# Optimization experiments

Hardware: AMD Instinct MI355X
Metric: run time of the kernel (lower is better)

## Reference

```python
import jax, jax.numpy as jnp
import numpy as np

H = 256  # GRU hidden size (self.dim)

def setup_inputs() -> dict:
    key = jax.random.key(0)
    ks = jax.random.split(key, 7)
    B, T, N_IN, N_C = 256, 512, 512, 101
    s_ih = 1.0 / np.sqrt(H)
    x    = jax.random.normal(ks[0], (B, T, N_IN), dtype=jnp.float32)
    W_ih = jax.random.uniform(ks[1], (3 * H, N_IN), minval=-s_ih, maxval=s_ih, dtype=jnp.float32)
    W_hh = jax.random.uniform(ks[2], (3 * H, H),    minval=-s_ih, maxval=s_ih, dtype=jnp.float32)
    b_ih = jax.random.uniform(ks[3], (3 * H,), minval=-s_ih, maxval=s_ih, dtype=jnp.float32)
    b_hh = jax.random.uniform(ks[4], (3 * H,), minval=-s_ih, maxval=s_ih, dtype=jnp.float32)
    s_fc = 1.0 / np.sqrt(H)
    fc_w = jax.random.uniform(ks[5], (N_C, H), minval=-s_fc, maxval=s_fc, dtype=jnp.float32)
    fc_b = jax.random.uniform(ks[6], (N_C,),   minval=-s_fc, maxval=s_fc, dtype=jnp.float32)
    return {"x": x, "W_ih": W_ih, "W_hh": W_hh, "b_ih": b_ih, "b_hh": b_hh,
            "fc_w": fc_w, "fc_b": fc_b}

def _gru_last_hidden(x, W_ih, W_hh, b_ih, b_hh):
    B = x.shape[0]
    # Precompute input-side gate projections for all timesteps: [B, T, 3H]
    xg = jnp.einsum('bti,gi->btg', x, W_ih) + b_ih
    h0 = jnp.zeros((B, H), dtype=x.dtype)

    def step(h, xg_t):
        hg = h @ W_hh.T + b_hh                      # [B, 3H]
        xr, xz, xn = jnp.split(xg_t, 3, axis=-1)    # PyTorch gate order: r, z, n
        hr, hz, hn = jnp.split(hg, 3, axis=-1)
        r = jax.nn.sigmoid(xr + hr)
        z = jax.nn.sigmoid(xz + hz)
        n = jnp.tanh(xn + r * hn)
        h_new = (1.0 - z) * n + z * h
        return h_new, None

    hT, _ = jax.lax.scan(step, h0, jnp.swapaxes(xg, 0, 1))  # scan over T
    return hT  # [B, H]

def reference(x, W_ih, W_hh, b_ih, b_hh, fc_w, fc_b):
    hT = _gru_last_hidden(x, W_ih, W_hh, b_ih, b_hh)
    return hT @ fc_w.T + fc_b  # [B, n_c]
```

## Files before the change

### kernel.cpp

```cpp
#include <hip/hip_runtime.h>
#include <hip/hip_bf16.h>
#include <cstdint>
#include <cstddef>

typedef __attribute__((ext_vector_type(4))) float floatx4;
typedef __attribute__((ext_vector_type(8))) short shortx8;
typedef __attribute__((ext_vector_type(2))) __fp16 f16x2;

#define T_SEQ 512
#define NIN   512
#define BATCH 256
#define HID   256
#define G3    768
#define NC    101

static __device__ __forceinline__ unsigned short f2bf(float f){
  unsigned int u = __float_as_uint(f);
  u += 0x7FFFu + ((u >> 16) & 1u);
  return (unsigned short)(u >> 16);
}

static __device__ __forceinline__ float dot2acc(f16x2 w, f16x2 h, float acc){
#if __has_builtin(__builtin_amdgcn_fdot2)
  return __builtin_amdgcn_fdot2(w, h, acc, false);
#else
  return acc + (float)w[0]*(float)h[0] + (float)w[1]*(float)h[1];
#endif
}

__global__ __launch_bounds__(256) void cvt_bf16(
    const float* __restrict__ src, unsigned short* __restrict__ dst, int n4)
{
  int i = blockIdx.x * 256 + threadIdx.x;
  const int stride = gridDim.x * 256;
  for (; i < n4; i += stride){
    const float4 v = *(const float4*)(src + (size_t)i * 4);
    union { unsigned short u[4]; uint2 q; } p;
    p.u[0] = f2bf(v.x); p.u[1] = f2bf(v.y); p.u[2] = f2bf(v.z); p.u[3] = f2bf(v.w);
    *(uint2*)(dst + (size_t)i * 4) = p.q;
  }
}

#define BM 128
#define BN 128
#define BK 64
#define LDK 72

__global__ __launch_bounds__(256) void gemm_xg(
    const unsigned short* __restrict__ xbf, const unsigned short* __restrict__ wbf,
    const float* __restrict__ bih, float* __restrict__ xg,
    int t0, int tcLog2)
{
  __shared__ unsigned short As[BM*LDK];
  __shared__ unsigned short Bs[BN*LDK];
  const int tid  = threadIdx.x;
  const int bn   = blockIdx.x;
  const int bm   = blockIdx.y;
  const int w    = tid >> 6;
  const int l    = tid & 63;
  const int lm   = l & 15;
  const int quad = l >> 4;

  const int srow2 = tid >> 3;
  const int scol8 = (tid & 7) * 8;
  const int tcMask = (1 << tcLog2) - 1;

  floatx4 acc[2][8];
  #pragma unroll
  for (int mt = 0; mt < 2; ++mt)
    #pragma unroll
    for (int nt = 0; nt < 8; ++nt)
      acc[mt][nt] = (floatx4){0.f, 0.f, 0.f, 0.f};

  for (int kt = 0; kt < NIN / BK; ++kt){
    const int k0 = kt * BK;
    __syncthreads();
    #pragma unroll
    for (int p = 0; p < 4; ++p){
      const int r  = p * 32 + srow2;
      const int gm = bm * BM + r;
      const int b  = gm >> tcLog2;
      const int tt = gm & tcMask;
      *(uint4*)&As[r * LDK + scol8] =
          *(const uint4*)(xbf + (size_t)(b * T_SEQ + t0 + tt) * NIN + k0 + scol8);
      const int gn = bn * BN + r;
      *(uint4*)&Bs[r * LDK + scol8] =
          *(const uint4*)(wbf + (size_t)gn * NIN + k0 + scol8);
    }
    __syncthreads();
    #pragma unroll
    for (int ks = 0; ks < 2; ++ks){
      const int kk = ks * 32 + quad * 8;
      shortx8 af[2], bfr[8];
      #pragma unroll
      for (int mt = 0; mt < 2; ++mt)
        af[mt] = *(const shortx8*)&As[(w * 32 + mt * 16 + lm) * LDK + kk];
      #pragma unroll
      for (int nt = 0; nt < 8; ++nt)
        bfr[nt] = *(const shortx8*)&Bs[(nt * 16 + lm) * LDK + kk];
      #pragma unroll
      for (int mt = 0; mt < 2; ++mt)
        #pragma unroll
        for (int nt = 0; nt < 8; ++nt)
          acc[mt][nt] = __builtin_amdgcn_mfma_f32_16x16x32_bf16(af[mt], bfr[nt], acc[mt][nt], 0, 0, 0);
    }
  }

  #pragma unroll
  for (int mt = 0; mt < 2; ++mt){
    #pragma unroll
    for (int nt = 0; nt < 8; ++nt){
      #pragma unroll
      for (int i = 0; i < 4; ++i){
        const int ml = w * 32 + mt * 16 + quad * 4 + i;
        const int nl = nt * 16 + lm;
        const int gm = bm * BM + ml;
        const int gn = bn * BN + nl;
        xg[(size_t)gm * G3 + gn] = acc[mt][nt][i] + bih[gn];
      }
    }
  }
}

#define HSTRIDE 280

__global__ __launch_bounds__(512, 2) void gru_steps(
    const float* __restrict__ xg, const float* __restrict__ Whh,
    const float* __restrict__ bhh, float* __restrict__ hstate, int Tc)
{
  __shared__ alignas(16) unsigned short hph[2][HSTRIDE];
  const int b    = blockIdx.x;
  const int tid  = threadIdx.x;
  const int j    = tid >> 1;
  const int half = tid & 1;
  const int jpos = j + (j >= 128 ? 8 : 0);

  f16x2 wrr[64], wrz[64], wrn[64];
  {
    const float4* r4 = (const float4*)(Whh + (size_t)j * HID + half * 128);
    const float4* z4 = (const float4*)(Whh + (size_t)(j + 256) * HID + half * 128);
    const float4* n4 = (const float4*)(Whh + (size_t)(j + 512) * HID + half * 128);
    #pragma unroll
    for (int k = 0; k < 32; ++k){
      float4 v = r4[k];
      wrr[2*k]   = __builtin_amdgcn_cvt_pkrtz(v.x, v.y);
      wrr[2*k+1] = __builtin_amdgcn_cvt_pkrtz(v.z, v.w);
    }
    #pragma unroll
    for (int k = 0; k < 32; ++k){
      float4 v = z4[k];
      wrz[2*k]   = __builtin_amdgcn_cvt_pkrtz(v.x, v.y);
      wrz[2*k+1] = __builtin_amdgcn_cvt_pkrtz(v.z, v.w);
    }
    #pragma unroll
    for (int k = 0; k < 32; ++k){
      float4 v = n4[k];
      wrn[2*k]   = __builtin_amdgcn_cvt_pkrtz(v.x, v.y);
      wrn[2*k+1] = __builtin_amdgcn_cvt_pkrtz(v.z, v.w);
    }
  }
  const float br = bhh[j];
  const float bz = bhh[j + 256];
  const float bn = bhh[j + 512];

  float hj = hstate[b * HID + j];
  if (half == 0){
    union { __fp16 f; unsigned short u; } cv;
    cv.f = (__fp16)hj;
    hph[0][jpos] = cv.u;
  }
  __syncthreads();

  const float* xgrow = xg + (size_t)b * Tc * G3 + j;
  float xr = xgrow[0], xz = xgrow[256], xn = xgrow[512];

  #pragma unroll 1
  for (int t = 0; t < Tc; ++t){
    const int tn = (t + 1 < Tc) ? (t + 1) : t;
    const float nxr = xgrow[(size_t)tn * G3];
    const float nxz = xgrow[(size_t)tn * G3 + 256];
    const float nxn = xgrow[(size_t)tn * G3 + 512];

    const uint4* hp4 = (const uint4*)(&hph[t & 1][0]) + half * 17;
    uint4 hv[16];
    #pragma unroll
    for (int i = 0; i < 16; ++i) hv[i] = hp4[i];

    float ar = 0.f, az = 0.f, an = 0.f;
    #pragma unroll
    for (int i = 0; i < 16; ++i){
      union { unsigned int u; f16x2 h; } c0, c1, c2, c3;
      c0.u = hv[i].x; c1.u = hv[i].y; c2.u = hv[i].z; c3.u = hv[i].w;
      const int p = 4 * i;
      ar = dot2acc(wrr[p    ], c0.h, ar);
      az = dot2acc(wrz[p    ], c0.h, az);
      an = dot2acc(wrn[p    ], c0.h, an);
      ar = dot2acc(wrr[p + 1], c1.h, ar);
      az = dot2acc(wrz[p + 1], c1.h, az);
      an = dot2acc(wrn[p + 1], c1.h, an);
      ar = dot2acc(wrr[p + 2], c2.h, ar);
      az = dot2acc(wrz[p + 2], c2.h, az);
      an = dot2acc(wrn[p + 2], c2.h, an);
      ar = dot2acc(wrr[p + 3], c3.h, ar);
      az = dot2acc(wrz[p + 3], c3.h, az);
      an = dot2acc(wrn[p + 3], c3.h, an);
    }
    const float hr = ar + __shfl_xor(ar, 1, 64) + br;
    const float hz = az + __shfl_xor(az, 1, 64) + bz;
    const float hn = an + __shfl_xor(an, 1, 64) + bn;

    const float r = 1.f / (1.f + __expf(-(xr + hr)));
    const float z = 1.f / (1.f + __expf(-(xz + hz)));
    const float a = xn + r * hn;
    const float ex = __expf(-2.f * fabsf(a));
    float n = (1.f - ex) / (1.f + ex);
    n = copysignf(n, a);
    const float hnew = fmaf(z, hj - n, n);

    hj = hnew;
    if (half == 0){
      union { __fp16 f; unsigned short u; } cv;
      cv.f = (__fp16)hj;
      hph[1 - (t & 1)][jpos] = cv.u;
    }
    __syncthreads();
    xr = nxr; xz = nxz; xn = nxn;
  }

  if (half == 0) hstate[b * HID + j] = hj;
}

__global__ __launch_bounds__(128) void fc_kernel(
    const float* __restrict__ hstate, const float* __restrict__ fw,
    const float* __restrict__ fb, float* __restrict__ out)
{
  __shared__ float hs[HID];
  const int b = blockIdx.x;
  const int t = threadIdx.x;
  hs[t]       = hstate[b * HID + t];
  hs[t + 128] = hstate[b * HID + t + 128];
  __syncthreads();
  if (t < NC){
    float acc = fb[t];
    const float4* w4 = (const float4*)(fw + (size_t)t * HID);
    const float4* h4 = (const float4*)hs;
    #pragma unroll
    for (int k = 0; k < 64; ++k){
      const float4 wv = w4[k];
      const float4 hv = h4[k];
      acc += wv.x * hv.x + wv.y * hv.y + wv.z * hv.z + wv.w * hv.w;
    }
    out[b * NC + t] = acc;
  }
}

extern "C" void kernel_launch(void* const* d_in, const int* in_sizes, int n_in,
                              void* d_out, int out_size, void* d_ws, size_t ws_size,
                              hipStream_t stream)
{
  const float* x   = (const float*)d_in[0];
  const float* Wih = (const float*)d_in[1];
  const float* Whh = (const float*)d_in[2];
  const float* bih = (const float*)d_in[3];
  const float* bhh = (const float*)d_in[4];
  const float* fcw = (const float*)d_in[5];
  const float* fcb = (const float*)d_in[6];
  float* out = (float*)d_out;

  const size_t hBytes   = (size_t)BATCH * HID * sizeof(float);
  const size_t xbfBytes = (size_t)BATCH * T_SEQ * NIN * 2;
  const size_t wbfBytes = (size_t)G3 * NIN * 2;
  float* hst = (float*)d_ws;
  unsigned short* xbf = (unsigned short*)((char*)d_ws + hBytes);
  unsigned short* wbf = (unsigned short*)((char*)d_ws + hBytes + xbfBytes);
  float* xg = (float*)((char*)d_ws + hBytes + xbfBytes + wbfBytes);

  const size_t fixed = hBytes + xbfBytes + wbfBytes;
  const size_t perT  = (size_t)BATCH * G3 * sizeof(float);
  const size_t avail = (ws_size > fixed) ? (ws_size - fixed) : 0;
  int tcLog2 = 9;
  while (tcLog2 > 0 && perT * ((size_t)1 << tcLog2) > avail) --tcLog2;
  const int Tc = 1 << tcLog2;

  cvt_bf16<<<2048, 256, 0, stream>>>(x, xbf, BATCH * T_SEQ * NIN / 4);
  cvt_bf16<<<384, 256, 0, stream>>>(Wih, wbf, G3 * NIN / 4);
  (void)hipMemsetAsync(hst, 0, hBytes, stream);
  for (int t0 = 0; t0 < T_SEQ; t0 += Tc){
    dim3 grid(6, 2 * Tc);
    gemm_xg<<<grid, 256, 0, stream>>>(xbf, wbf, bih, xg, t0, tcLog2);
    gru_steps<<<BATCH, 512, 0, stream>>>(xg, Whh, bhh, hst, Tc);
  }
  fc_kernel<<<BATCH, 128, 0, stream>>>(hst, fcw, fcb, out);
}
```

Before: 1.272 ms.

## Split GRU hidden dot products across four lanes with DPP reduction

The recurrent step kernel now runs 1024 threads per block instead of 512, so each hidden unit's three gate dot products are split across four lanes of 64 elements each rather than two lanes of 128. The cross-lane partial sums are combined with two DPP quad-permute adds in place of ds_swizzle shuffles. The shared-memory padding is adjusted so each quarter of h is read from its own bank-offset region. This halves per-thread register weights and serial FMA chain length per timestep, at the cost of more waves sharing the barrier and more redundant h loads and gate math per unit.

Measured after the change: 1.360 ms. +6.9%, slower.

```diff
diff --git a/kernel.cpp b/kernel.cpp
--- a/kernel.cpp
+++ b/kernel.cpp
@@ -26,6 +26,12 @@
 #else
   return acc + (float)w[0]*(float)h[0] + (float)w[1]*(float)h[1];
 #endif
+}
+
+template<int CTRL>
+static __device__ __forceinline__ float dppadd(float v){
+  return v + __int_as_float(__builtin_amdgcn_update_dpp(
+      0, __float_as_int(v), CTRL, 0xF, 0xF, true));
 }
 
 __global__ __launch_bounds__(256) void cvt_bf16(
@@ -124,39 +130,40 @@
 
 #define HSTRIDE 280
 
-__global__ __launch_bounds__(512, 2) void gru_steps(
+__global__ __attribute__((amdgpu_flat_work_group_size(1024, 1024), amdgpu_waves_per_eu(4, 4)))
+void gru_steps(
     const float* __restrict__ xg, const float* __restrict__ Whh,
     const float* __restrict__ bhh, float* __restrict__ hstate, int Tc)
 {
   __shared__ alignas(16) unsigned short hph[2][HSTRIDE];
-  const int b    = blockIdx.x;
-  const int tid  = threadIdx.x;
-  const int j    = tid >> 1;
-  const int half = tid & 1;
-  const int jpos = j + (j >= 128 ? 8 : 0);
-
-  f16x2 wrr[64], wrz[64], wrn[64];
+  const int b   = blockIdx.x;
+  const int tid = threadIdx.x;
+  const int j   = tid >> 2;
+  const int q   = tid & 3;
+  const int jpos = j + ((j >> 6) << 3);
+
+  f16x2 wr[32], wz[32], wn[32];
   {
-    const float4* r4 = (const float4*)(Whh + (size_t)j * HID + half * 128);
-    const float4* z4 = (const float4*)(Whh + (size_t)(j + 256) * HID + half * 128);
-    const float4* n4 = (const float4*)(Whh + (size_t)(j + 512) * HID + half * 128);
-    #pragma unroll
-    for (int k = 0; k < 32; ++k){
+    const float4* r4 = (const float4*)(Whh + (size_t)j * HID + q * 64);
+    const float4* z4 = (const float4*)(Whh + (size_t)(j + 256) * HID + q * 64);
+    const float4* n4 = (const float4*)(Whh + (size_t)(j + 512) * HID + q * 64);
+    #pragma unroll
+    for (int k = 0; k < 16; ++k){
       float4 v = r4[k];
-      wrr[2*k]   = __builtin_amdgcn_cvt_pkrtz(v.x, v.y);
-      wrr[2*k+1] = __builtin_amdgcn_cvt_pkrtz(v.z, v.w);
-    }
-    #pragma unroll
-    for (int k = 0; k < 32; ++k){
+      wr[2*k]   = __builtin_amdgcn_cvt_pkrtz(v.x, v.y);
+      wr[2*k+1] = __builtin_amdgcn_cvt_pkrtz(v.z, v.w);
+    }
+    #pragma unroll
+    for (int k = 0; k < 16; ++k){
       float4 v = z4[k];
-      wrz[2*k]   = __builtin_amdgcn_cvt_pkrtz(v.x, v.y);
-      wrz[2*k+1] = __builtin_amdgcn_cvt_pkrtz(v.z, v.w);
-    }
-    #pragma unroll
-    for (int k = 0; k < 32; ++k){
+      wz[2*k]   = __builtin_amdgcn_cvt_pkrtz(v.x, v.y);
+      wz[2*k+1] = __builtin_amdgcn_cvt_pkrtz(v.z, v.w);
+    }
+    #pragma unroll
+    for (int k = 0; k < 16; ++k){
       float4 v = n4[k];
-      wrn[2*k]   = __builtin_amdgcn_cvt_pkrtz(v.x, v.y);
-      wrn[2*k+1] = __builtin_amdgcn_cvt_pkrtz(v.z, v.w);
+      wn[2*k]   = __builtin_amdgcn_cvt_pkrtz(v.x, v.y);
+      wn[2*k+1] = __builtin_amdgcn_cvt_pkrtz(v.z, v.w);
     }
   }
   const float br = bhh[j];
@@ -164,7 +171,7 @@
   const float bn = bhh[j + 512];
 
   float hj = hstate[b * HID + j];
-  if (half == 0){
+  if (q == 0){
     union { __fp16 f; unsigned short u; } cv;
     cv.f = (__fp16)hj;
     hph[0][jpos] = cv.u;
@@ -181,33 +188,40 @@
     const float nxz = xgrow[(size_t)tn * G3 + 256];
     const float nxn = xgrow[(size_t)tn * G3 + 512];
 
-    const uint4* hp4 = (const uint4*)(&hph[t & 1][0]) + half * 17;
-    uint4 hv[16];
-    #pragma unroll
-    for (int i = 0; i < 16; ++i) hv[i] = hp4[i];
+    const uint4* hp4 = (const uint4*)(&hph[t & 1][0]) + 9 * q;
 
     float ar = 0.f, az = 0.f, an = 0.f;
     #pragma unroll
-    for (int i = 0; i < 16; ++i){
-      union { unsigned int u; f16x2 h; } c0, c1, c2, c3;
-      c0.u = hv[i].x; c1.u = hv[i].y; c2.u = hv[i].z; c3.u = hv[i].w;
-      const int p = 4 * i;
-      ar = dot2acc(wrr[p    ], c0.h, ar);
-      az = dot2acc(wrz[p    ], c0.h, az);
-      an = dot2acc(wrn[p    ], c0.h, an);
-      ar = dot2acc(wrr[p + 1], c1.h, ar);
-      az = dot2acc(wrz[p + 1], c1.h, az);
-      an = dot2acc(wrn[p + 1], c1.h, an);
-      ar = dot2acc(wrr[p + 2], c2.h, ar);
-      az = dot2acc(wrz[p + 2], c2.h, az);
-      an = dot2acc(wrn[p + 2], c2.h, an);
-      ar = dot2acc(wrr[p + 3], c3.h, ar);
-      az = dot2acc(wrz[p + 3], c3.h, az);
-      an = dot2acc(wrn[p + 3], c3.h, an);
-    }
-    const float hr = ar + __shfl_xor(ar, 1, 64) + br;
-    const float hz = az + __shfl_xor(az, 1, 64) + bz;
-    const float hn = an + __shfl_xor(an, 1, 64) + bn;
+    for (int hb = 0; hb < 2; ++hb){
+      uint4 hv[4];
+      #pragma unroll
+      for (int i = 0; i < 4; ++i) hv[i] = hp4[hb * 4 + i];
+      #pragma unroll
+      for (int i = 0; i < 4; ++i){
+        union { unsigned int u; f16x2 h; } c0, c1, c2, c3;
+        c0.u = hv[i].x; c1.u = hv[i].y; c2.u = hv[i].z; c3.u = hv[i].w;
+        const int p = hb * 16 + 4 * i;
+        ar = dot2acc(wr[p    ], c0.h, ar);
+        az = dot2acc(wz[p    ], c0.h, az);
+        an = dot2acc(wn[p    ], c0.h, an);
+        ar = dot2acc(wr[p + 1], c1.h, ar);
+        az = dot2acc(wz[p + 1], c1.h, az);
+        an = dot2acc(wn[p + 1], c1.h, an);
+        ar = dot2acc(wr[p + 2], c2.h, ar);
+        az = dot2acc(wz[p + 2], c2.h, az);
+        an = dot2acc(wn[p + 2], c2.h, an);
+        ar = dot2acc(wr[p + 3], c3.h, ar);
+        az = dot2acc(wz[p + 3], c3.h, az);
+        an = dot2acc(wn[p + 3], c3.h, an);
+      }
+    }
+
+    ar = dppadd<0xB1>(ar); az = dppadd<0xB1>(az); an = dppadd<0xB1>(an);
+    ar = dppadd<0x4E>(ar); az = dppadd<0x4E>(az); an = dppadd<0x4E>(an);
+
+    const float hr = ar + br;
+    const float hz = az + bz;
+    const float hn = an + bn;
 
     const float r = 1.f / (1.f + __expf(-(xr + hr)));
     const float z = 1.f / (1.f + __expf(-(xz + hz)));
@@ -218,7 +232,7 @@
     const float hnew = fmaf(z, hj - n, n);
 
     hj = hnew;
-    if (half == 0){
+    if (q == 0){
       union { __fp16 f; unsigned short u; } cv;
       cv.f = (__fp16)hj;
       hph[1 - (t & 1)][jpos] = cv.u;
@@ -227,7 +241,7 @@
     xr = nxr; xz = nxz; xn = nxn;
   }
 
-  if (half == 0) hstate[b * HID + j] = hj;
+  if (q == 0) hstate[b * HID + j] = hj;
 }
 
 __global__ __launch_bounds__(128) void fc_kernel(
@@ -288,7 +302,7 @@
   for (int t0 = 0; t0 < T_SEQ; t0 += Tc){
     dim3 grid(6, 2 * Tc);
     gemm_xg<<<grid, 256, 0, stream>>>(xbf, wbf, bih, xg, t0, tcLog2);
-    gru_steps<<<BATCH, 512, 0, stream>>>(xg, Whh, bhh, hst, Tc);
+    gru_steps<<<BATCH, 1024, 0, stream>>>(xg, Whh, bhh, hst, Tc);
   }
   fc_kernel<<<BATCH, 128, 0, stream>>>(hst, fcw, fcb, out);
 }
```
